# Optimization experiments

Hardware: AMD Instinct MI355X
Metric: run time of the kernel (lower is better)

Reference implementation:

```python
import jax, jax.numpy as jnp
import numpy as np

B, T, D = 32, 2048, 80
K1 = K2 = 3
S1 = S2 = 2
CB_DIM, CB_SIZE = 512, 1024
MASK_P = 0.1
NOISE_STD = 0.1
INPUT_DIM = D * K1 * K2  # 720


def _win_idx(T_in, k, s):
    Tp = (T_in - k) // s + 1
    return jnp.arange(Tp)[:, None] * s + jnp.arange(k)[None, :]  # (Tp, k)


def _unfold(x, k, s):
    # matches torch x.unfold(1, k, s).view(B, Tp, -1): out[b, t, f*k + j] = x[b, t*s + j, f]
    idx = _win_idx(x.shape[1], k, s)
    w = x[:, idx, :]                 # (B, Tp, k, F)
    w = jnp.swapaxes(w, 2, 3)        # (B, Tp, F, k)
    return w.reshape(w.shape[0], w.shape[1], -1)


def setup_inputs() -> dict:
    key = jax.random.key(0)
    k1, k2, k3, k4, k5 = jax.random.split(key, 5)
    raw_feats = jax.random.normal(k1, (B, T, D), jnp.float32)
    auged_feats = jax.random.normal(k2, (B, T, D), jnp.float32)
    length = jax.random.randint(k3, (B,), T // 2, T + 1)
    xav = (2.0 / (INPUT_DIM + CB_DIM)) ** 0.5  # xavier_normal std
    projector = jax.random.normal(k4, (INPUT_DIM, CB_DIM), jnp.float32) * xav
    codebook = jax.random.normal(k5, (CB_SIZE, CB_DIM), jnp.float32)
    return {"raw_feats": raw_feats, "auged_feats": auged_feats, "length": length,
            "projector": projector, "codebook": codebook}


def reference(raw_feats, auged_feats, length, projector, codebook):
    T1 = (T - K1) // S1 + 1
    T2 = (T1 - K2) // S2 + 1
    idx1 = _win_idx(T, K1, S1)                         # (T1, K1)
    idx2 = _win_idx(T1, K2, S2)                        # (T2, K2)
    frame_windows = idx1[idx2].reshape(T2, K1 * K2)    # (T2, 9) original frame idx per subsampled step
    label_lengths = ((length - K1) // S1 + 1 - K2) // S2 + 1  # (B,)

    # --- label path: two torch-style unfolds -> project -> nearest codebook entry ---
    stacked = _unfold(_unfold(raw_feats, K1, S1), K2, S2)     # (B, T2, 720)
    targets = jnp.matmul(stacked, projector)                  # (B, T2, 512)
    # squared-euclidean expansion; same argmin as ||t - c||
    dist = (jnp.sum(targets * targets, axis=-1, keepdims=True)
            - 2.0 * jnp.einsum('btd,cd->btc', targets, codebook)
            + jnp.sum(codebook * codebook, axis=-1))          # (B, T2, 1024)
    labels = jnp.argmin(dist, axis=-1) + 1                    # labels start from 1; 0 = ignore idx
    valid = jnp.arange(T2)[None, :] < label_lengths[:, None]  # (B, T2)
    labels = jnp.where(valid, labels, 0)[None]                # (num_codebooks=1, B, T2)

    # --- static (span length 1) random masking on valid subsampled steps ---
    mkey = jax.random.key(42)
    km, kn = jax.random.split(mkey)
    masked = (jax.random.uniform(km, (B, T2)) < MASK_P) & valid
    masked_dim = masked.astype(jnp.float32)                   # (B, T2)
    # scatter masked subsampled steps back onto original frame indices (union of windows)
    hits = jnp.zeros((B, T), jnp.float32).at[:, frame_windows].add(masked_dim[:, :, None])
    frame_mask = hits > 0                                     # (B, T)
    noise = NOISE_STD * jax.random.normal(kn, (B, T, D), auged_feats.dtype)
    masked_feats = jnp.where(frame_mask[:, :, None], noise, auged_feats)
    return masked_feats, labels, masked_dim
```

## Files before the change

### kernel.cpp

```cpp
#include <hip/hip_runtime.h>
#include <cstdint>

#define B_    32
#define T_    2048
#define D_    80
#define T2_   511
#define NROW  16352
#define GK    720
#define CBD   512
#define CBS   1024
#define HMASK 8176
#define HN    2621440
#define NP    16384
#define KB    23

using bfrag = __attribute__((ext_vector_type(8))) short;
using f32x4 = __attribute__((ext_vector_type(4))) float;
using s4    = __attribute__((ext_vector_type(4))) short;

__device__ inline ushort f2bf(float f){
  uint32_t u = __float_as_uint(f);
  uint32_t r = (u + 0x7FFFu + ((u >> 16) & 1u)) >> 16;
  return (ushort)r;
}
__device__ inline float bf2f(ushort h){ return __uint_as_float(((uint32_t)h) << 16); }

#define GLL16(gsrc, ldst) __builtin_amdgcn_global_load_lds( \
    (__attribute__((address_space(1))) void*)(gsrc), \
    (__attribute__((address_space(3))) void*)(ldst), 16, 0, 0)

__host__ __device__ inline uint32_t rotl_(uint32_t v, int d){ return (v<<d)|(v>>(32-d)); }

__host__ __device__ inline void tf2x32(uint32_t k0, uint32_t k1, uint32_t& x0, uint32_t& x1){
  uint32_t ks2 = k0 ^ k1 ^ 0x1BD11BDAu;
  x0 += k0; x1 += k1;
  const int r0[4] = {13,15,26,6}, r1[4] = {17,29,16,24};
#pragma unroll
  for (int i=0;i<4;i++){ x0 += x1; x1 = rotl_(x1, r0[i]); x1 ^= x0; }
  x0 += k1; x1 += ks2 + 1u;
#pragma unroll
  for (int i=0;i<4;i++){ x0 += x1; x1 = rotl_(x1, r1[i]); x1 ^= x0; }
  x0 += ks2; x1 += k0 + 2u;
#pragma unroll
  for (int i=0;i<4;i++){ x0 += x1; x1 = rotl_(x1, r0[i]); x1 ^= x0; }
  x0 += k0; x1 += k1 + 3u;
#pragma unroll
  for (int i=0;i<4;i++){ x0 += x1; x1 = rotl_(x1, r1[i]); x1 ^= x0; }
  x0 += k1; x1 += ks2 + 4u;
#pragma unroll
  for (int i=0;i<4;i++){ x0 += x1; x1 = rotl_(x1, r0[i]); x1 ^= x0; }
  x0 += ks2; x1 += k0 + 5u;
}

__device__ inline float erfinv_f(float x){
  float w = -log1pf(-x*x);
  float p;
  if (w < 5.0f){
    w -= 2.5f;
    p = 2.81022636e-08f;
    p = fmaf(p, w, 3.43273939e-07f);
    p = fmaf(p, w, -3.5233877e-06f);
    p = fmaf(p, w, -4.39150654e-06f);
    p = fmaf(p, w, 0.00021858087f);
    p = fmaf(p, w, -0.00125372503f);
    p = fmaf(p, w, -0.00417768164f);
    p = fmaf(p, w, 0.246640727f);
    p = fmaf(p, w, 1.50140941f);
  } else {
    w = sqrtf(w) - 3.0f;
    p = -0.000200214257f;
    p = fmaf(p, w, 0.000100950558f);
    p = fmaf(p, w, 0.00134934322f);
    p = fmaf(p, w, -0.00367342844f);
    p = fmaf(p, w, 0.00573950773f);
    p = fmaf(p, w, -0.0076224613f);
    p = fmaf(p, w, 0.00943887047f);
    p = fmaf(p, w, 1.00167406f);
    p = fmaf(p, w, 2.83297682f);
  }
  return p * x;
}

__device__ inline int label_len(int L){ return (((L - 3) / 2) - 2) / 2 + 1; }

__global__ void cbnorm_k(const float* __restrict__ cb, ushort* __restrict__ W0, ushort* __restrict__ W1){
  int c = blockIdx.x, lane = threadIdx.x;
  double s = 0.0;
  for (int k = lane; k < CBD; k += 64){ float v = cb[c*CBD + k]; s += (double)v * (double)v; }
#pragma unroll
  for (int off = 32; off; off >>= 1) s += __shfl_down(s, off);
  float nf = (float)s;
  nf = __shfl(nf, 0);
  size_t base = ((size_t)(KB-1)*CBS + c)*32;
  if (lane == 16){
    float h = -0.5f * nf;
    ushort h0 = f2bf(h); ushort h1 = f2bf(h - bf2f(h0));
    W0[base+16] = h0; W1[base+16] = h1;
  } else if (lane > 16 && lane < 32){
    W0[base+lane] = 0; W1[base+lane] = 0;
  }
}

__global__ void gather_k(const float* __restrict__ raw, ushort* __restrict__ S0, ushort* __restrict__ S1){
  int idx4 = blockIdx.x * 256 + threadIdx.x;
  int kk4 = idx4 & 7;
  int n   = (idx4 >> 3) & (NP - 1);
  int kb  = idx4 >> 17;
  int b = n / T2_, t2 = n - b * T2_;
  s4 o0, o1;
#pragma unroll
  for (int j = 0; j < 4; ++j){
    int k = kb*32 + kk4*4 + j;
    float v = 0.f;
    if (n < NROW){
      if (k < GK){
        int d = k / 9, rem = k - 9*d;
        int k1 = rem / 3, k2 = rem - 3*k1;
        int tm = 4*t2 + 2*k2 + k1;
        v = raw[(b * T_ + tm) * D_ + d];
      } else if (k == GK) v = 1.f;
    }
    ushort h0 = f2bf(v); ushort h1 = f2bf(v - bf2f(h0));
    o0[j] = (short)h0; o1[j] = (short)h1;
  }
  size_t off = ((size_t)kb*NP + n)*32 + kk4*4;
  *(s4*)&S0[off] = o0;
  *(s4*)&S1[off] = o1;
}

__global__ __launch_bounds__(256) void wgemm_k(const float* __restrict__ P, const float* __restrict__ cb,
                                               ushort* __restrict__ W0, ushort* __restrict__ W1){
  __shared__ float sP[16][68];
  __shared__ float sC[16][68];
  int r0 = blockIdx.y * 64, c0 = blockIdx.x * 64;
  int tid = threadIdx.x, tx = tid & 15, ty = tid >> 4;
  float acc[4][4] = {};
  for (int k0 = 0; k0 < CBD; k0 += 16){
    __syncthreads();
    {
      int r = tid >> 2, kq = tid & 3;
      int rr = r0 + r;
      float4 v = {0.f,0.f,0.f,0.f};
      if (rr < GK) v = *(const float4*)&P[rr * CBD + k0 + kq * 4];
      sP[kq*4+0][r] = v.x; sP[kq*4+1][r] = v.y; sP[kq*4+2][r] = v.z; sP[kq*4+3][r] = v.w;
      float4 w = *(const float4*)&cb[(c0 + r) * CBD + k0 + kq * 4];
      sC[kq*4+0][r] = w.x; sC[kq*4+1][r] = w.y; sC[kq*4+2][r] = w.z; sC[kq*4+3][r] = w.w;
    }
    __syncthreads();
#pragma unroll
    for (int kk = 0; kk < 16; ++kk){
      float4 a = *(const float4*)&sP[kk][ty * 4];
      float4 b = *(const float4*)&sC[kk][tx * 4];
      float av[4] = {a.x,a.y,a.z,a.w}, bv[4] = {b.x,b.y,b.z,b.w};
#pragma unroll
      for (int i = 0; i < 4; ++i)
#pragma unroll
        for (int j = 0; j < 4; ++j) acc[i][j] = fmaf(av[i], bv[j], acc[i][j]);
    }
  }
#pragma unroll
  for (int i = 0; i < 4; ++i){
    int r = r0 + ty * 4 + i;
    if (r < GK){
#pragma unroll
      for (int j = 0; j < 4; ++j){
        int c = c0 + tx * 4 + j;
        float v = acc[i][j];
        ushort h0 = f2bf(v); ushort h1 = f2bf(v - bf2f(h0));
        size_t o = ((size_t)(r >> 5) * CBS + c) * 32 + (r & 31);
        W0[o] = h0; W1[o] = h1;
      }
    }
  }
}

__global__ __launch_bounds__(256) void score_k(const ushort* __restrict__ S0, const ushort* __restrict__ S1,
                                               const ushort* __restrict__ W0, const ushort* __restrict__ W1,
                                               float* __restrict__ pval, int* __restrict__ pidx){
  __shared__ __align__(16) ushort lA[2][128*32];
  __shared__ __align__(16) ushort lB[2][128*32];
  int tid = threadIdx.x;
  int lane = tid & 63, wid = tid >> 6;
  int wm = wid >> 1, wn = wid & 1;
  int g = lane >> 4, lr = lane & 15;
  int n0 = blockIdx.y * 128, c0 = blockIdx.x * 128;
  f32x4 acc[4][4] = {};
  for (int kb = 0; kb < KB; ++kb){
    const ushort* src; ushort* dst;
    if      (wid == 0){ src = S0 + ((size_t)kb*NP  + n0)*32; dst = &lA[0][0]; }
    else if (wid == 1){ src = S1 + ((size_t)kb*NP  + n0)*32; dst = &lA[1][0]; }
    else if (wid == 2){ src = W0 + ((size_t)kb*CBS + c0)*32; dst = &lB[0][0]; }
    else              { src = W1 + ((size_t)kb*CBS + c0)*32; dst = &lB[1][0]; }
    __syncthreads();
#pragma unroll
    for (int q = 0; q < 8; ++q)
      GLL16(src + q*512 + lane*8, dst + q*512);
    __syncthreads();
    bfrag a[2][4], bfr[2][4];
#pragma unroll
    for (int mt = 0; mt < 4; ++mt){
      int m = wm*64 + mt*16 + lr;
      a[0][mt] = *(const bfrag*)&lA[0][m*32 + g*8];
      a[1][mt] = *(const bfrag*)&lA[1][m*32 + g*8];
    }
#pragma unroll
    for (int nt = 0; nt < 4; ++nt){
      int c = wn*64 + nt*16 + lr;
      bfr[0][nt] = *(const bfrag*)&lB[0][c*32 + g*8];
      bfr[1][nt] = *(const bfrag*)&lB[1][c*32 + g*8];
    }
#pragma unroll
    for (int mt = 0; mt < 4; ++mt)
#pragma unroll
      for (int nt = 0; nt < 4; ++nt){
        acc[mt][nt] = __builtin_amdgcn_mfma_f32_16x16x32_bf16(a[0][mt], bfr[0][nt], acc[mt][nt], 0,0,0);
        acc[mt][nt] = __builtin_amdgcn_mfma_f32_16x16x32_bf16(a[0][mt], bfr[1][nt], acc[mt][nt], 0,0,0);
        acc[mt][nt] = __builtin_amdgcn_mfma_f32_16x16x32_bf16(a[1][mt], bfr[0][nt], acc[mt][nt], 0,0,0);
      }
  }
  float bv[4][4]; int bi[4][4];
#pragma unroll
  for (int mt = 0; mt < 4; ++mt)
#pragma unroll
    for (int r = 0; r < 4; ++r){
      float best = 3.4e38f; int besti = 0;
#pragma unroll
      for (int nt = 0; nt < 4; ++nt){
        float d = -2.f * acc[mt][nt][r];
        int c = c0 + wn*64 + nt*16 + lr;
        if (d < best){ best = d; besti = c; }
      }
      bv[mt][r] = best; bi[mt][r] = besti;
    }
#pragma unroll
  for (int off = 1; off < 16; off <<= 1){
#pragma unroll
    for (int mt = 0; mt < 4; ++mt)
#pragma unroll
      for (int r = 0; r < 4; ++r){
        float ov = __shfl_xor(bv[mt][r], off);
        int   oi = __shfl_xor(bi[mt][r], off);
        if (ov < bv[mt][r] || (ov == bv[mt][r] && oi < bi[mt][r])){ bv[mt][r] = ov; bi[mt][r] = oi; }
      }
  }
  if (lr == 0){
    int p = blockIdx.x*2 + wn;
#pragma unroll
    for (int mt = 0; mt < 4; ++mt)
#pragma unroll
      for (int r = 0; r < 4; ++r){
        int n = n0 + wm*64 + mt*16 + g*4 + r;
        pval[(size_t)p*NP + n] = bv[mt][r];
        pidx[(size_t)p*NP + n] = bi[mt][r];
      }
  }
}

__global__ void combine_k(const float* __restrict__ pval, const int* __restrict__ pidx,
                          const int* __restrict__ len, float* __restrict__ lb){
  int n = blockIdx.x * 256 + threadIdx.x;
  if (n >= NROW) return;
  float bv = pval[n]; int bi = pidx[n];
#pragma unroll
  for (int p = 1; p < 16; ++p){
    float v = pval[(size_t)p*NP + n]; int ii = pidx[(size_t)p*NP + n];
    if (v < bv || (v == bv && ii < bi)){ bv = v; bi = ii; }
  }
  int b = n / T2_, t2 = n - b * T2_;
  lb[n] = (t2 < label_len(len[b])) ? (float)(bi + 1) : 0.f;
}

__device__ inline void emit_mask(const int* len, float* md, int i, uint32_t bits){
  float u = __uint_as_float((bits >> 9) | 0x3F800000u) - 1.0f;
  int b = i / T2_, t2 = i - b * T2_;
  bool m = (u < 0.1f) && (t2 < label_len(len[b]));
  md[i] = m ? 1.0f : 0.0f;
}

__global__ void mask_k(const int* __restrict__ len, float* __restrict__ md, uint32_t km0, uint32_t km1){
  int j = blockIdx.x * 256 + threadIdx.x;
  if (j >= HMASK) return;
  uint32_t x0 = (uint32_t)j, x1 = (uint32_t)(j + HMASK);
  tf2x32(km0, km1, x0, x1);
  emit_mask(len, md, j, x0);
  emit_mask(len, md, j + HMASK, x1);
}

__device__ inline void emit_feat(const float* aug, const float* md, float* mf, int i, uint32_t bits){
  int tabs = i / D_;
  int t = tabs & (T_ - 1);
  int b = i / (D_ * T_);
  int lo = (t < 3) ? 0 : ((t - 3) >> 2);
  int hi = t >> 2; if (hi > T2_ - 1) hi = T2_ - 1;
  bool m = false;
  for (int t2 = lo; t2 <= hi; ++t2) m = m || (md[b * T2_ + t2] != 0.f);
  float v;
  if (m){
    float f = __uint_as_float((bits >> 9) | 0x3F800000u) - 1.0f;
    const float LOV = -0.99999994f;
    float u = fmaf(f, 2.0f, LOV);
    u = fmaxf(LOV, u);
    v = 0.1f * (1.41421356f * erfinv_f(u));
  } else {
    v = aug[i];
  }
  mf[i] = v;
}

__global__ void feats_k(const float* __restrict__ aug, const float* __restrict__ md,
                        float* __restrict__ mf, uint32_t kn0, uint32_t kn1){
  int j = blockIdx.x * 256 + threadIdx.x;
  uint32_t x0 = (uint32_t)j, x1 = (uint32_t)(j + HN);
  tf2x32(kn0, kn1, x0, x1);
  emit_feat(aug, md, mf, j, x0);
  emit_feat(aug, md, mf, j + HN, x1);
}

extern "C" void kernel_launch(void* const* d_in, const int* in_sizes, int n_in,
                              void* d_out, int out_size, void* d_ws, size_t ws_size,
                              hipStream_t stream){
  const float* raw  = (const float*)d_in[0];
  const float* aug  = (const float*)d_in[1];
  const int*   len  = (const int*)  d_in[2];
  const float* proj = (const float*)d_in[3];
  const float* cb   = (const float*)d_in[4];

  float* out = (float*)d_out;
  float* mf  = out;
  float* lb  = out + 5242880;
  float* md  = out + 5259232;

  ushort* w  = (ushort*)d_ws;
  ushort* W0 = w;
  ushort* W1 = W0 + (size_t)KB*CBS*32;
  ushort* S0 = W1 + (size_t)KB*CBS*32;
  ushort* S1 = S0 + (size_t)KB*NP*32;
  float* pval = (float*)(S1 + (size_t)KB*NP*32);
  int*   pidx = (int*)(pval + (size_t)16*NP);

  uint32_t a0 = 0u, a1 = 2u, b0 = 1u, b1 = 3u;
  tf2x32(0u, 42u, a0, a1);
  tf2x32(0u, 42u, b0, b1);
  uint32_t km0 = a0, km1 = b0, kn0 = a1, kn1 = b1;

  cbnorm_k<<<CBS, 64, 0, stream>>>(cb, W0, W1);
  wgemm_k<<<dim3(CBS / 64, 12), 256, 0, stream>>>(proj, cb, W0, W1);
  gather_k<<<(KB * NP * 8) / 256, 256, 0, stream>>>(raw, S0, S1);
  score_k<<<dim3(CBS / 128, NP / 128), 256, 0, stream>>>(S0, S1, W0, W1, pval, pidx);
  combine_k<<<(NROW + 255) / 256, 256, 0, stream>>>(pval, pidx, len, lb);
  mask_k<<<(HMASK + 255) / 256, 256, 0, stream>>>(len, md, km0, km1);
  feats_k<<<HN / 256, 256, 0, stream>>>(aug, md, mf, kn0, kn1);
}
```

Baseline: 179.5 us.

## Double-buffer score GEMM, swizzle LDS layout, split-K projector GEMM, remap blocks per XCD

The score kernel now double-buffers its LDS tiles so the next K-block's global-to-LDS loads overlap the current MFMAs, with one barrier per iteration. Operand layouts in S and W are XOR-swizzled to avoid LDS bank conflicts on fragment reads. The grid is flattened and remapped so that the blocks of each XCD share row tiles for L2 reuse. The projector-codebook GEMM is split four ways along K, with a new reduction kernel, to expose more parallelism. The cost is doubled LDS use, which may lower occupancy, plus an extra kernel launch and a workspace buffer.

```diff
diff --git a/kernel.cpp b/kernel.cpp
--- a/kernel.cpp
+++ b/kernel.cpp
@@ -92,12 +92,13 @@
   float nf = (float)s;
   nf = __shfl(nf, 0);
   size_t base = ((size_t)(KB-1)*CBS + c)*32;
+  int sw = ((c >> 1) & 3) << 3;
   if (lane == 16){
     float h = -0.5f * nf;
     ushort h0 = f2bf(h); ushort h1 = f2bf(h - bf2f(h0));
-    W0[base+16] = h0; W1[base+16] = h1;
+    W0[base + (16 ^ sw)] = h0; W1[base + (16 ^ sw)] = h1;
   } else if (lane > 16 && lane < 32){
-    W0[base+lane] = 0; W1[base+lane] = 0;
+    W0[base + (lane ^ sw)] = 0; W1[base + (lane ^ sw)] = 0;
   }
 }
 
@@ -123,19 +124,21 @@
     ushort h0 = f2bf(v); ushort h1 = f2bf(v - bf2f(h0));
     o0[j] = (short)h0; o1[j] = (short)h1;
   }
-  size_t off = ((size_t)kb*NP + n)*32 + kk4*4;
+  int kk4s = kk4 ^ ((((n >> 1)) & 3) << 1);
+  size_t off = ((size_t)kb*NP + n)*32 + kk4s*4;
   *(s4*)&S0[off] = o0;
   *(s4*)&S1[off] = o1;
 }
 
 __global__ __launch_bounds__(256) void wgemm_k(const float* __restrict__ P, const float* __restrict__ cb,
-                                               ushort* __restrict__ W0, ushort* __restrict__ W1){
+                                               float* __restrict__ Wp){
   __shared__ float sP[16][68];
   __shared__ float sC[16][68];
   int r0 = blockIdx.y * 64, c0 = blockIdx.x * 64;
+  int kz = blockIdx.z;
   int tid = threadIdx.x, tx = tid & 15, ty = tid >> 4;
   float acc[4][4] = {};
-  for (int k0 = 0; k0 < CBD; k0 += 16){
+  for (int k0 = kz * 128; k0 < kz * 128 + 128; k0 += 16){
     __syncthreads();
     {
       int r = tid >> 2, kq = tid & 3;
@@ -162,52 +165,77 @@
   for (int i = 0; i < 4; ++i){
     int r = r0 + ty * 4 + i;
     if (r < GK){
-#pragma unroll
-      for (int j = 0; j < 4; ++j){
-        int c = c0 + tx * 4 + j;
-        float v = acc[i][j];
-        ushort h0 = f2bf(v); ushort h1 = f2bf(v - bf2f(h0));
-        size_t o = ((size_t)(r >> 5) * CBS + c) * 32 + (r & 31);
-        W0[o] = h0; W1[o] = h1;
-      }
-    }
-  }
+      float4 o; o.x = acc[i][0]; o.y = acc[i][1]; o.z = acc[i][2]; o.w = acc[i][3];
+      *(float4*)&Wp[((size_t)kz * GK + r) * CBS + c0 + tx * 4] = o;
+    }
+  }
+}
+
+__global__ void wreduce_k(const float* __restrict__ Wp, ushort* __restrict__ W0, ushort* __restrict__ W1){
+  int idx = blockIdx.x * 256 + threadIdx.x;
+  int r = idx >> 10, c = idx & (CBS - 1);
+  float v = Wp[(size_t)r * CBS + c]
+          + Wp[((size_t)GK + r) * CBS + c]
+          + Wp[((size_t)2*GK + r) * CBS + c]
+          + Wp[((size_t)3*GK + r) * CBS + c];
+  ushort h0 = f2bf(v); ushort h1 = f2bf(v - bf2f(h0));
+  size_t o = ((size_t)(r >> 5) * CBS + c) * 32 + ((r & 31) ^ (((c >> 1) & 3) << 3));
+  W0[o] = h0; W1[o] = h1;
 }
 
 __global__ __launch_bounds__(256) void score_k(const ushort* __restrict__ S0, const ushort* __restrict__ S1,
                                                const ushort* __restrict__ W0, const ushort* __restrict__ W1,
                                                float* __restrict__ pval, int* __restrict__ pidx){
-  __shared__ __align__(16) ushort lA[2][128*32];
-  __shared__ __align__(16) ushort lB[2][128*32];
+  __shared__ __align__(16) ushort lA[2][2][128*32];
+  __shared__ __align__(16) ushort lB[2][2][128*32];
   int tid = threadIdx.x;
   int lane = tid & 63, wid = tid >> 6;
   int wm = wid >> 1, wn = wid & 1;
   int g = lane >> 4, lr = lane & 15;
-  int n0 = blockIdx.y * 128, c0 = blockIdx.x * 128;
+  int id = blockIdx.x;
+  int xcd = id & 7, slot = id >> 3;
+  int cidx = slot & 7, ridx = (xcd << 4) | (slot >> 3);
+  int n0 = ridx * 128, c0 = cidx * 128;
+
+  const ushort* base;
+  size_t stride32;
+  if      (wid == 0){ base = S0 + (size_t)n0*32; stride32 = (size_t)NP*32; }
+  else if (wid == 1){ base = S1 + (size_t)n0*32; stride32 = (size_t)NP*32; }
+  else if (wid == 2){ base = W0 + (size_t)c0*32; stride32 = (size_t)CBS*32; }
+  else              { base = W1 + (size_t)c0*32; stride32 = (size_t)CBS*32; }
+  ushort* dstA[2] = { &lA[0][wid&1][0], &lA[1][wid&1][0] };
+  ushort* dstB[2] = { &lB[0][wid&1][0], &lB[1][wid&1][0] };
+
   f32x4 acc[4][4] = {};
+  {
+    const ushort* src = base;
+    ushort* dst = (wid < 2) ? dstA[0] : dstB[0];
+#pragma unroll
+    for (int q = 0; q < 8; ++q) GLL16(src + q*512 + lane*8, dst + q*512);
+  }
+  __syncthreads();
+  int buf = 0;
   for (int kb = 0; kb < KB; ++kb){
-    const ushort* src; ushort* dst;
-    if      (wid == 0){ src = S0 + ((size_t)kb*NP  + n0)*32; dst = &lA[0][0]; }
-    else if (wid == 1){ src = S1 + ((size_t)kb*NP  + n0)*32; dst = &lA[1][0]; }
-    else if (wid == 2){ src = W0 + ((size_t)kb*CBS + c0)*32; dst = &lB[0][0]; }
-    else              { src = W1 + ((size_t)kb*CBS + c0)*32; dst = &lB[1][0]; }
-    __syncthreads();
-#pragma unroll
-    for (int q = 0; q < 8; ++q)
-      GLL16(src + q*512 + lane*8, dst + q*512);
-    __syncthreads();
+    if (kb + 1 < KB){
+      const ushort* src = base + (size_t)(kb+1) * stride32;
+      ushort* dst = (wid < 2) ? dstA[buf^1] : dstB[buf^1];
+#pragma unroll
+      for (int q = 0; q < 8; ++q) GLL16(src + q*512 + lane*8, dst + q*512);
+    }
     bfrag a[2][4], bfr[2][4];
 #pragma unroll
     for (int mt = 0; mt < 4; ++mt){
       int m = wm*64 + mt*16 + lr;
-      a[0][mt] = *(const bfrag*)&lA[0][m*32 + g*8];
-      a[1][mt] = *(const bfrag*)&lA[1][m*32 + g*8];
+      int sw = (g ^ ((m >> 1) & 3)) * 8;
+      a[0][mt] = *(const bfrag*)&lA[buf][0][m*32 + sw];
+      a[1][mt] = *(const bfrag*)&lA[buf][1][m*32 + sw];
     }
 #pragma unroll
     for (int nt = 0; nt < 4; ++nt){
       int c = wn*64 + nt*16 + lr;
-      bfr[0][nt] = *(const bfrag*)&lB[0][c*32 + g*8];
-      bfr[1][nt] = *(const bfrag*)&lB[1][c*32 + g*8];
+      int sw = (g ^ ((c >> 1) & 3)) * 8;
+      bfr[0][nt] = *(const bfrag*)&lB[buf][0][c*32 + sw];
+      bfr[1][nt] = *(const bfrag*)&lB[buf][1][c*32 + sw];
     }
 #pragma unroll
     for (int mt = 0; mt < 4; ++mt)
@@ -217,6 +245,8 @@
         acc[mt][nt] = __builtin_amdgcn_mfma_f32_16x16x32_bf16(a[0][mt], bfr[1][nt], acc[mt][nt], 0,0,0);
         acc[mt][nt] = __builtin_amdgcn_mfma_f32_16x16x32_bf16(a[1][mt], bfr[0][nt], acc[mt][nt], 0,0,0);
       }
+    __syncthreads();
+    buf ^= 1;
   }
   float bv[4][4]; int bi[4][4];
 #pragma unroll
@@ -244,7 +274,7 @@
       }
   }
   if (lr == 0){
-    int p = blockIdx.x*2 + wn;
+    int p = cidx*2 + wn;
 #pragma unroll
     for (int mt = 0; mt < 4; ++mt)
 #pragma unroll
@@ -337,6 +367,7 @@
   ushort* S1 = S0 + (size_t)KB*NP*32;
   float* pval = (float*)(S1 + (size_t)KB*NP*32);
   int*   pidx = (int*)(pval + (size_t)16*NP);
+  float* Wp   = (float*)(pidx + (size_t)16*NP);
 
   uint32_t a0 = 0u, a1 = 2u, b0 = 1u, b1 = 3u;
   tf2x32(0u, 42u, a0, a1);
@@ -344,9 +375,10 @@
   uint32_t km0 = a0, km1 = b0, kn0 = a1, kn1 = b1;
 
   cbnorm_k<<<CBS, 64, 0, stream>>>(cb, W0, W1);
-  wgemm_k<<<dim3(CBS / 64, 12), 256, 0, stream>>>(proj, cb, W0, W1);
+  wgemm_k<<<dim3(CBS / 64, 12, 4), 256, 0, stream>>>(proj, cb, Wp);
+  wreduce_k<<<(GK * CBS) / 256, 256, 0, stream>>>(Wp, W0, W1);
   gather_k<<<(KB * NP * 8) / 256, 256, 0, stream>>>(raw, S0, S1);
-  score_k<<<dim3(CBS / 128, NP / 128), 256, 0, stream>>>(S0, S1, W0, W1, pval, pidx);
+  score_k<<<1024, 256, 0, stream>>>(S0, S1, W0, W1, pval, pidx);
   combine_k<<<(NROW + 255) / 256, 256, 0, stream>>>(pval, pidx, len, lb);
   mask_k<<<(HMASK + 255) / 256, 256, 0, stream>>>(len, md, km0, km1);
   feats_k<<<HN / 256, 256, 0, stream>>>(aug, md, mf, kn0, kn1);
```

After: 161.0 us. 10.3% less time.
